# Optimization experiments

Hardware: AMD Instinct MI355X
Metric: run time of the kernel (lower is better)

Reference implementation:

```python
import jax, jax.numpy as jnp
import numpy as np

N = 4096   # node_each_graph == in_feats (adjacency-row node features)
H = 512    # n_hidden
C = 2      # n_classes
E = 65536  # edges (avg degree 16)
NL = 5     # n_layers -> 4 GINConv layers
NR = NL - 2  # stacked hidden GIN layers (layers 1..3)


def _bn(x, g, b, m, v):
    # BatchNorm1d in eval mode (running stats), eps=1e-5
    return (x - m) * jax.lax.rsqrt(v + 1e-5) * g + b


def setup_inputs():
    key = jax.random.key(0)
    ks = iter(jax.random.split(key, 16))
    nk = lambda: next(ks)
    s = 0.02
    f32 = jnp.float32
    d = {}
    d["feat"] = jax.random.normal(nk(), (N, N), f32)
    d["edge_src"] = jax.random.randint(nk(), (E,), 0, N)
    d["edge_dst"] = jax.random.randint(nk(), (E,), 0, N)
    # GIN layer 0: MLP is Linear(N,H)-BN-ReLU-Linear(H,H); ApplyNodeFunc BN; outer BN
    d["eps0"] = jnp.zeros((), f32)
    d["W0a"] = jax.random.normal(nk(), (N, H), f32) * s
    d["b0a"] = jnp.zeros((H,), f32)
    d["W0b"] = jax.random.normal(nk(), (H, H), f32) * s
    d["b0b"] = jnp.zeros((H,), f32)
    for nm in ["bn0a", "bnA0", "bnO0"]:
        d[nm + "_g"] = jnp.ones((H,), f32); d[nm + "_b"] = jnp.zeros((H,), f32)
        d[nm + "_m"] = jnp.zeros((H,), f32); d[nm + "_v"] = jnp.ones((H,), f32)
    # GIN layers 1..NL-2 stacked (H -> H)
    d["epsR"] = jnp.zeros((NR,), f32)
    d["WRa"] = jax.random.normal(nk(), (NR, H, H), f32) * s
    d["bRa"] = jnp.zeros((NR, H), f32)
    d["WRb"] = jax.random.normal(nk(), (NR, H, H), f32) * s
    d["bRb"] = jnp.zeros((NR, H), f32)
    for nm in ["bnRa", "bnAR", "bnOR"]:
        d[nm + "_g"] = jnp.ones((NR, H), f32); d[nm + "_b"] = jnp.zeros((NR, H), f32)
        d[nm + "_m"] = jnp.zeros((NR, H), f32); d[nm + "_v"] = jnp.ones((NR, H), f32)
    # per-hidden-rep readout linears (batch_size = 1)
    d["Wp0"] = jax.random.normal(nk(), (N * N, C), f32) * 0.001
    d["bp0"] = jnp.zeros((C,), f32)
    d["WpR"] = jax.random.normal(nk(), (NL - 1, N * H, C), f32) * 0.001
    d["bpR"] = jnp.zeros((NL - 1, C), f32)
    return d


def _gin(h, src, dst, eps, Wa, ba, bna, Wb, bb, bnA, bnO):
    # GINConv sum-aggregation: (1+eps)*h + sum over in-neighbors
    agg = jax.ops.segment_sum(h[src], dst, num_segments=N)
    x = (1.0 + eps) * h + agg
    # MLP (num_layers=2): Linear -> BN -> ReLU -> Linear
    x = jax.nn.relu(_bn(x @ Wa + ba, *bna))
    x = x @ Wb + bb
    # ApplyNodeFunc: BN -> ReLU
    x = jax.nn.relu(_bn(x, *bnA))
    # Model-level BN -> ReLU
    x = jax.nn.relu(_bn(x, *bnO))
    return x


def reference(feat, edge_src, edge_dst, eps0, W0a, b0a, W0b, b0b,
              bn0a_g, bn0a_b, bn0a_m, bn0a_v, bnA0_g, bnA0_b, bnA0_m, bnA0_v,
              bnO0_g, bnO0_b, bnO0_m, bnO0_v,
              epsR, WRa, bRa, WRb, bRb,
              bnRa_g, bnRa_b, bnRa_m, bnRa_v, bnAR_g, bnAR_b, bnAR_m, bnAR_v,
              bnOR_g, bnOR_b, bnOR_m, bnOR_v, Wp0, bp0, WpR, bpR):
    h = _gin(feat, edge_src, edge_dst, eps0, W0a, b0a,
             (bn0a_g, bn0a_b, bn0a_m, bn0a_v), W0b, b0b,
             (bnA0_g, bnA0_b, bnA0_m, bnA0_v), (bnO0_g, bnO0_b, bnO0_m, bnO0_v))
    hs = [h]
    for i in range(NR):  # small fixed layer loop
        h = _gin(h, edge_src, edge_dst, epsR[i], WRa[i], bRa[i],
                 (bnRa_g[i], bnRa_b[i], bnRa_m[i], bnRa_v[i]), WRb[i], bRb[i],
                 (bnAR_g[i], bnAR_b[i], bnAR_m[i], bnAR_v[i]),
                 (bnOR_g[i], bnOR_b[i], bnOR_m[i], bnOR_v[i]))
        hs.append(h)
    # jumping-knowledge readout over hidden_rep (eval: dropout = identity)
    score = feat.reshape(1, -1) @ Wp0 + bp0
    for i, hi in enumerate(hs):
        score = score + hi.reshape(1, -1) @ WpR[i] + bpR[i]
    return score
```

## Files before the change

kernel.cpp:

```cpp
#include <hip/hip_runtime.h>
#include <cstdint>
#include <cstddef>

typedef __attribute__((ext_vector_type(8))) short short8;
typedef __attribute__((ext_vector_type(4))) float f32x4;
typedef __attribute__((ext_vector_type(4))) float f4;
typedef __attribute__((ext_vector_type(2))) float f2;
typedef __attribute__((ext_vector_type(4))) unsigned short us4;

#define NN 4096
#define HH 512
#define EE 65536

#define GLOAD(gp, lp) __builtin_amdgcn_global_load_lds( \
    (const __attribute__((address_space(1))) void*)(gp), \
    (__attribute__((address_space(3))) void*)(lp), 16, 0, 0)

__device__ __forceinline__ unsigned short f2bf(float x) {
    union { float f; unsigned u; } un; un.f = x;
    unsigned r = un.u + 0x7fffu + ((un.u >> 16) & 1u);
    return (unsigned short)(r >> 16);
}
__device__ __forceinline__ float b2f(unsigned short v) {
    union { unsigned u; float f; } un; un.u = ((unsigned)v) << 16; return un.f;
}

__global__ __launch_bounds__(1024) void k_histscan(const int* __restrict__ edst,
                                                   int* __restrict__ starts) {
    __shared__ int cnt[NN];
    __shared__ int wtot[16], woff[16];
    const int t = threadIdx.x;
    for (int i = t; i < NN; i += 1024) cnt[i] = 0;
    __syncthreads();
    for (int i = t; i < EE; i += 1024) atomicAdd(&cnt[edst[i]], 1);
    __syncthreads();
    const int b = t * 4;
    const int c0 = cnt[b], c1 = cnt[b + 1], c2 = cnt[b + 2], c3 = cnt[b + 3];
    const int s = c0 + c1 + c2 + c3;
    const int lane = t & 63, wv = t >> 6;
    int inc = s;
    for (int d = 1; d < 64; d <<= 1) {
        int v = __shfl_up(inc, d);
        if (lane >= d) inc += v;
    }
    if (lane == 63) wtot[wv] = inc;
    __syncthreads();
    if (t == 0) {
        int a = 0;
        for (int i = 0; i < 16; ++i) { woff[i] = a; a += wtot[i]; }
        starts[NN] = a;
    }
    __syncthreads();
    int run = woff[wv] + inc - s;
    starts[b] = run; run += c0;
    starts[b + 1] = run; run += c1;
    starts[b + 2] = run; run += c2;
    starts[b + 3] = run;
}

__global__ void k_scatter(const int* __restrict__ src, const int* __restrict__ dst,
                          const int* __restrict__ starts, int* __restrict__ cursor,
                          int* __restrict__ sorted) {
    int e = blockIdx.x * 256 + threadIdx.x;
    if (e < EE) {
        int d = dst[e];
        int p = starts[d] + atomicAdd(&cursor[d], 1);
        sorted[p] = src[e];
    }
}

__global__ void k_binsort(const int* __restrict__ starts, int* __restrict__ a) {
    int d = blockIdx.x * 256 + threadIdx.x;
    if (d < NN) {
        int s = starts[d], e = starts[d + 1];
        for (int i = s + 1; i < e; ++i) {
            int v = a[i]; int j = i - 1;
            while (j >= s && a[j] > v) { a[j + 1] = a[j]; --j; }
            a[j + 1] = v;
        }
    }
}

__global__ __launch_bounds__(256) void k_cvtdot0(const float* __restrict__ feat,
                                                 const float* __restrict__ w,
                                                 unsigned short* __restrict__ featb,
                                                 float* __restrict__ part) {
    __shared__ f4 fs[1024];
    __shared__ float s0[256], s1[256];
    const int t = threadIdx.x;
    const long B0 = (long)blockIdx.x * 1024;
    const f4* ff = (const f4*)feat;
    const f4* ww = (const f4*)w;
    f4 v[4];
#pragma unroll
    for (int k = 0; k < 4; ++k)
        v[k] = __builtin_nontemporal_load(ff + B0 + k * 256 + t);
#pragma unroll
    for (int k = 0; k < 4; ++k) {
        fs[k * 256 + t] = v[k];
        us4 o;
        o.x = f2bf(v[k].x); o.y = f2bf(v[k].y); o.z = f2bf(v[k].z); o.w = f2bf(v[k].w);
        ((us4*)featb)[B0 + k * 256 + t] = o;
    }
    f4 wv[8];
#pragma unroll
    for (int k = 0; k < 8; ++k)
        wv[k] = __builtin_nontemporal_load(ww + 2 * B0 + k * 256 + t);
    __syncthreads();
    float a0 = 0.f, a1 = 0.f;
#pragma unroll
    for (int k = 0; k < 8; ++k) {
        const int q = k * 256 + t;
        f2 fp = *(const f2*)((const char*)fs + (size_t)q * 8);
        a0 += fp.x * wv[k].x + fp.y * wv[k].z;
        a1 += fp.x * wv[k].y + fp.y * wv[k].w;
    }
    s0[t] = a0; s1[t] = a1;
    __syncthreads();
    for (int s = 128; s > 0; s >>= 1) {
        if (t < s) { s0[t] += s0[t + s]; s1[t] += s1[t + s]; }
        __syncthreads();
    }
    if (t == 0) { part[2 * blockIdx.x] = s0[0]; part[2 * blockIdx.x + 1] = s1[0]; }
}

__global__ __launch_bounds__(256) void k_transcvt8(const float* __restrict__ W0a,
                                                   const float* __restrict__ W0b,
                                                   const float* __restrict__ WRa,
                                                   const float* __restrict__ WRb,
                                                   unsigned short* __restrict__ w0at,
                                                   unsigned short* __restrict__ wt) {
    __shared__ float tile[32][33];
    const int z = blockIdx.z;
    const float* W;
    unsigned short* Wt;
    int K;
    if (z == 7) {
        W = W0a; Wt = w0at; K = NN;
    } else {
        if (blockIdx.x >= 16 || blockIdx.y >= 16) return;
        W = (z == 0) ? W0b : (z < 4) ? WRa + (size_t)(z - 1) * HH * HH
                                     : WRb + (size_t)(z - 4) * HH * HH;
        Wt = wt + (size_t)z * HH * HH; K = HH;
    }
    const int k0 = blockIdx.x * 32, n0 = blockIdx.y * 32;
    const int tx = threadIdx.x & 31, ty = threadIdx.x >> 5;
    for (int r = ty; r < 32; r += 8)
        tile[r][tx] = W[(size_t)(k0 + r) * HH + n0 + tx];
    __syncthreads();
    for (int r = ty; r < 32; r += 8)
        Wt[(size_t)(n0 + r) * K + k0 + tx] = f2bf(tile[tx][r]);
}

__global__ __launch_bounds__(256) void k_gemm0(
    const unsigned short* __restrict__ A, const unsigned short* __restrict__ Bt,
    int M, int N, int K, float* __restrict__ outf)
{
    __shared__ alignas(16) unsigned short As[2][128 * 32];
    __shared__ alignas(16) unsigned short Bs[2][128 * 32];
    const int t = threadIdx.x;
    const int lane = t & 63, w = t >> 6;
    const int wr = w >> 1, wc = w & 1;
    const int l15 = lane & 15, l4 = lane >> 4;
    const int m0 = blockIdx.x * 128, n0 = blockIdx.y * 128;

    f32x4 acc[4][4];
#pragma unroll
    for (int i = 0; i < 4; ++i)
#pragma unroll
        for (int j = 0; j < 4; ++j) acc[i][j] = (f32x4){0.f, 0.f, 0.f, 0.f};

    const int Kc = K / gridDim.z;
    const int kbase = blockIdx.z * Kc;
    const unsigned short* ga0 = A + (size_t)m0 * K + kbase + (size_t)(t >> 2) * K + (t & 3) * 8;
    const unsigned short* ga1 = ga0 + (size_t)64 * K;
    const unsigned short* gb0 = Bt + (size_t)n0 * K + kbase + (size_t)(t >> 2) * K + (t & 3) * 8;
    const unsigned short* gb1 = gb0 + (size_t)64 * K;

    auto stage = [&](int kt, int buf) {
        const int ko = kt * 32;
        GLOAD(ga0 + ko, &As[buf][t * 8]);
        GLOAD(ga1 + ko, &As[buf][(t + 256) * 8]);
        GLOAD(gb0 + ko, &Bs[buf][t * 8]);
        GLOAD(gb1 + ko, &Bs[buf][(t + 256) * 8]);
    };

    const int nk = Kc >> 5;
    stage(0, 0);
    __syncthreads();
    for (int kt = 0; kt < nk; ++kt) {
        const int cur = kt & 1;
        if (kt + 1 < nk) stage(kt + 1, cur ^ 1);
        short8 aF[4], bF[4];
#pragma unroll
        for (int i = 0; i < 4; ++i)
            aF[i] = *(const short8*)(&As[cur][(wr * 64 + i * 16 + l15) * 32 + 8 * l4]);
#pragma unroll
        for (int j = 0; j < 4; ++j)
            bF[j] = *(const short8*)(&Bs[cur][(wc * 64 + j * 16 + l15) * 32 + 8 * l4]);
#pragma unroll
        for (int i = 0; i < 4; ++i)
#pragma unroll
            for (int j = 0; j < 4; ++j)
                acc[i][j] = __builtin_amdgcn_mfma_f32_16x16x32_bf16(aF[i], bF[j], acc[i][j], 0, 0, 0);
        __syncthreads();
    }

    const int mrow = m0 + wr * 64;
    float* op = outf + (size_t)blockIdx.z * M * N;
#pragma unroll
    for (int j = 0; j < 4; ++j) {
        const int cg = n0 + wc * 64 + j * 16 + l15;
#pragma unroll
        for (int i = 0; i < 4; ++i)
#pragma unroll
            for (int r = 0; r < 4; ++r)
                op[(size_t)(mrow + i * 16 + l4 * 4 + r) * N + cg] = acc[i][j][r];
    }
}

template<int EPI, bool DOT>
__global__ __launch_bounds__(512) void k_gemmH(
    const unsigned short* __restrict__ A, const unsigned short* __restrict__ Bt,
    const float* __restrict__ bias,
    const float* __restrict__ g1p, const float* __restrict__ b1p,
    const float* __restrict__ m1p, const float* __restrict__ v1p,
    const float* __restrict__ g2p, const float* __restrict__ b2p,
    const float* __restrict__ m2p, const float* __restrict__ v2p,
    unsigned short* __restrict__ outb,
    const float* __restrict__ wq, float* __restrict__ part, int slotbase)
{
    constexpr int K = HH, N = HH;
    __shared__ alignas(16) unsigned short As[2][128 * 32];
    __shared__ alignas(16) unsigned short Bs[2][64 * 32];
    const int t = threadIdx.x;
    const int lane = t & 63, w = t >> 6;
    const int wr = w >> 1, wc = w & 1;
    const int l15 = lane & 15, l4 = lane >> 4;
    const int m0 = blockIdx.x * 128, n0 = blockIdx.y * 64;

    f32x4 acc[2][2];
#pragma unroll
    for (int i = 0; i < 2; ++i)
#pragma unroll
        for (int j = 0; j < 2; ++j) acc[i][j] = (f32x4){0.f, 0.f, 0.f, 0.f};

    const unsigned short* ga = A + (size_t)m0 * K + (size_t)(t >> 2) * K + (t & 3) * 8;
    const unsigned short* gb = Bt + (size_t)n0 * K + (size_t)(t >> 2) * K + (t & 3) * 8;

    auto stage = [&](int kt, int buf) {
        const int ko = kt * 32;
        GLOAD(ga + ko, &As[buf][t * 8]);
        if (t < 256) GLOAD(gb + ko, &Bs[buf][t * 8]);
    };

    const int nk = K >> 5;
    stage(0, 0);
    __syncthreads();
    for (int kt = 0; kt < nk; ++kt) {
        const int cur = kt & 1;
        if (kt + 1 < nk) stage(kt + 1, cur ^ 1);
        short8 aF[2], bF[2];
#pragma unroll
        for (int i = 0; i < 2; ++i)
            aF[i] = *(const short8*)(&As[cur][(wr * 32 + i * 16 + l15) * 32 + 8 * l4]);
#pragma unroll
        for (int j = 0; j < 2; ++j)
            bF[j] = *(const short8*)(&Bs[cur][(wc * 32 + j * 16 + l15) * 32 + 8 * l4]);
#pragma unroll
        for (int i = 0; i < 2; ++i)
#pragma unroll
            for (int j = 0; j < 2; ++j)
                acc[i][j] = __builtin_amdgcn_mfma_f32_16x16x32_bf16(aF[i], bF[j], acc[i][j], 0, 0, 0);
        __syncthreads();
    }

    const int mrow = m0 + wr * 32;
    float d0 = 0.f, d1 = 0.f;
#pragma unroll
    for (int j = 0; j < 2; ++j) {
        const int cg = n0 + wc * 32 + j * 16 + l15;
        const float bi = bias[cg];
        const float sc1 = rsqrtf(v1p[cg] + 1e-5f) * g1p[cg];
        const float sh1 = b1p[cg] - m1p[cg] * sc1;
        float sc2 = 1.f, sh2 = 0.f;
        if (EPI == 3) {
            sc2 = rsqrtf(v2p[cg] + 1e-5f) * g2p[cg];
            sh2 = b2p[cg] - m2p[cg] * sc2;
        }
#pragma unroll
        for (int i = 0; i < 2; ++i) {
#pragma unroll
            for (int r = 0; r < 4; ++r) {
                const int rg = mrow + i * 16 + l4 * 4 + r;
                float x = acc[i][j][r];
                x = fmaxf((x + bi) * sc1 + sh1, 0.f);
                if (EPI == 3) x = fmaxf(x * sc2 + sh2, 0.f);
                outb[(size_t)rg * N + cg] = f2bf(x);
                if constexpr (DOT) {
                    float2 wvv = ((const float2*)wq)[(size_t)rg * N + cg];
                    d0 += x * wvv.x; d1 += x * wvv.y;
                }
            }
        }
    }
    if constexpr (DOT) {
        __shared__ float r0[512], r1[512];
        r0[t] = d0; r1[t] = d1;
        __syncthreads();
        for (int s = 256; s > 0; s >>= 1) {
            if (t < s) { r0[t] += r0[t + s]; r1[t] += r1[t + s]; }
            __syncthreads();
        }
        if (t == 0) {
            const int slot = slotbase + blockIdx.y * gridDim.x + blockIdx.x;
            part[2 * slot] = r0[0]; part[2 * slot + 1] = r1[0];
        }
    }
}

__global__ __launch_bounds__(256) void k_red4b(const float* __restrict__ p,
                                               unsigned short* __restrict__ G0b) {
    const long S = (long)NN * HH / 4;
    long i = blockIdx.x * 256L + threadIdx.x;
    float4 a = ((const float4*)p)[i];
    float4 b = ((const float4*)p)[i + S];
    float4 c = ((const float4*)p)[i + 2 * S];
    float4 d = ((const float4*)p)[i + 3 * S];
    us4 o;
    o.x = f2bf((a.x + b.x) + (c.x + d.x));
    o.y = f2bf((a.y + b.y) + (c.y + d.y));
    o.z = f2bf((a.z + b.z) + (c.z + d.z));
    o.w = f2bf((a.w + b.w) + (c.w + d.w));
    ((us4*)G0b)[i] = o;
}

__global__ __launch_bounds__(128) void k_agg0(
    const unsigned short* __restrict__ G0, const int* __restrict__ starts,
    const int* __restrict__ sorted, const float* __restrict__ epsp,
    const float* __restrict__ bias,
    const float* __restrict__ bg, const float* __restrict__ bb,
    const float* __restrict__ bm, const float* __restrict__ bv,
    unsigned short* __restrict__ outb)
{
    const int d = blockIdx.x, t = threadIdx.x;
    const float ep = 1.0f + epsp[0];
    ushort4 ow = ((const ushort4*)(G0 + (size_t)d * HH))[t];
    float sx = 0.f, sy = 0.f, sz = 0.f, sw = 0.f;
    const int e0 = starts[d], e1 = starts[d + 1];
    int i = e0;
    for (; i + 4 <= e1; i += 4) {
        int q0 = sorted[i], q1 = sorted[i + 1], q2 = sorted[i + 2], q3 = sorted[i + 3];
        ushort4 x0 = ((const ushort4*)(G0 + (size_t)q0 * HH))[t];
        ushort4 x1 = ((const ushort4*)(G0 + (size_t)q1 * HH))[t];
        ushort4 x2 = ((const ushort4*)(G0 + (size_t)q2 * HH))[t];
        ushort4 x3 = ((const ushort4*)(G0 + (size_t)q3 * HH))[t];
        sx += (b2f(x0.x) + b2f(x1.x)) + (b2f(x2.x) + b2f(x3.x));
        sy += (b2f(x0.y) + b2f(x1.y)) + (b2f(x2.y) + b2f(x3.y));
        sz += (b2f(x0.z) + b2f(x1.z)) + (b2f(x2.z) + b2f(x3.z));
        sw += (b2f(x0.w) + b2f(x1.w)) + (b2f(x2.w) + b2f(x3.w));
    }
    for (; i < e1; ++i) {
        ushort4 x = ((const ushort4*)(G0 + (size_t)sorted[i] * HH))[t];
        sx += b2f(x.x); sy += b2f(x.y); sz += b2f(x.z); sw += b2f(x.w);
    }
    float4 bi = ((const float4*)bias)[t];
    float4 g4 = ((const float4*)bg)[t];
    float4 b4 = ((const float4*)bb)[t];
    float4 m4 = ((const float4*)bm)[t];
    float4 v4 = ((const float4*)bv)[t];
    float x0 = ep * b2f(ow.x) + sx + bi.x;
    float x1 = ep * b2f(ow.y) + sy + bi.y;
    float x2 = ep * b2f(ow.z) + sz + bi.z;
    float x3 = ep * b2f(ow.w) + sw + bi.w;
    x0 = fmaxf((x0 - m4.x) * rsqrtf(v4.x + 1e-5f) * g4.x + b4.x, 0.f);
    x1 = fmaxf((x1 - m4.y) * rsqrtf(v4.y + 1e-5f) * g4.y + b4.y, 0.f);
    x2 = fmaxf((x2 - m4.z) * rsqrtf(v4.z + 1e-5f) * g4.z + b4.z, 0.f);
    x3 = fmaxf((x3 - m4.w) * rsqrtf(v4.w + 1e-5f) * g4.w + b4.w, 0.f);
    ushort4 o; o.x = f2bf(x0); o.y = f2bf(x1); o.z = f2bf(x2); o.w = f2bf(x3);
    ((ushort4*)(outb + (size_t)d * HH))[t] = o;
}

__global__ __launch_bounds__(128) void k_aggL(
    const unsigned short* __restrict__ hsrc, const int* __restrict__ starts,
    const int* __restrict__ sorted, const float* __restrict__ epsp,
    unsigned short* __restrict__ outb)
{
    const int d = blockIdx.x, t = threadIdx.x;
    const float ep = 1.0f + epsp[0];
    ushort4 ow = ((const ushort4*)(hsrc + (size_t)d * HH))[t];
    float sx = 0.f, sy = 0.f, sz = 0.f, sw = 0.f;
    const int e0 = starts[d], e1 = starts[d + 1];
    int i = e0;
    for (; i + 4 <= e1; i += 4) {
        int q0 = sorted[i], q1 = sorted[i + 1], q2 = sorted[i + 2], q3 = sorted[i + 3];
        ushort4 x0 = ((const ushort4*)(hsrc + (size_t)q0 * HH))[t];
        ushort4 x1 = ((const ushort4*)(hsrc + (size_t)q1 * HH))[t];
        ushort4 x2 = ((const ushort4*)(hsrc + (size_t)q2 * HH))[t];
        ushort4 x3 = ((const ushort4*)(hsrc + (size_t)q3 * HH))[t];
        sx += (b2f(x0.x) + b2f(x1.x)) + (b2f(x2.x) + b2f(x3.x));
        sy += (b2f(x0.y) + b2f(x1.y)) + (b2f(x2.y) + b2f(x3.y));
        sz += (b2f(x0.z) + b2f(x1.z)) + (b2f(x2.z) + b2f(x3.z));
        sw += (b2f(x0.w) + b2f(x1.w)) + (b2f(x2.w) + b2f(x3.w));
    }
    for (; i < e1; ++i) {
        ushort4 x = ((const ushort4*)(hsrc + (size_t)sorted[i] * HH))[t];
        sx += b2f(x.x); sy += b2f(x.y); sz += b2f(x.z); sw += b2f(x.w);
    }
    ushort4 o;
    o.x = f2bf(ep * b2f(ow.x) + sx);
    o.y = f2bf(ep * b2f(ow.y) + sy);
    o.z = f2bf(ep * b2f(ow.z) + sz);
    o.w = f2bf(ep * b2f(ow.w) + sw);
    ((ushort4*)(outb + (size_t)d * HH))[t] = o;
}

__global__ __launch_bounds__(256) void k_final(const float* __restrict__ part, int nslot,
                                               const float* __restrict__ bp0, const float* __restrict__ bpR,
                                               float* __restrict__ out) {
    __shared__ float s0[256], s1[256];
    int t = threadIdx.x;
    float a0 = 0.f, a1 = 0.f;
    for (int i = t; i < nslot; i += 256) { a0 += part[2 * i]; a1 += part[2 * i + 1]; }
    s0[t] = a0; s1[t] = a1;
    __syncthreads();
    for (int s = 128; s > 0; s >>= 1) {
        if (t < s) { s0[t] += s0[t + s]; s1[t] += s1[t + s]; }
        __syncthreads();
    }
    if (t == 0) {
        out[0] = s0[0] + bp0[0] + bpR[0] + bpR[2] + bpR[4] + bpR[6];
        out[1] = s1[0] + bp0[1] + bpR[1] + bpR[3] + bpR[5] + bpR[7];
    }
}

extern "C" void kernel_launch(void* const* d_in, const int* in_sizes, int n_in,
                              void* d_out, int out_size, void* d_ws, size_t ws_size,
                              hipStream_t stream)
{
    const float* feat = (const float*)d_in[0];
    const int*   esrc = (const int*)d_in[1];
    const int*   edst = (const int*)d_in[2];
    const float* eps0 = (const float*)d_in[3];
    const float* W0a  = (const float*)d_in[4];
    const float* b0a  = (const float*)d_in[5];
    const float* W0b  = (const float*)d_in[6];
    const float* b0b  = (const float*)d_in[7];
    const float* bn0a_g = (const float*)d_in[8];
    const float* bn0a_b = (const float*)d_in[9];
    const float* bn0a_m = (const float*)d_in[10];
    const float* bn0a_v = (const float*)d_in[11];
    const float* bnA0_g = (const float*)d_in[12];
    const float* bnA0_b = (const float*)d_in[13];
    const float* bnA0_m = (const float*)d_in[14];
    const float* bnA0_v = (const float*)d_in[15];
    const float* bnO0_g = (const float*)d_in[16];
    const float* bnO0_b = (const float*)d_in[17];
    const float* bnO0_m = (const float*)d_in[18];
    const float* bnO0_v = (const float*)d_in[19];
    const float* epsR = (const float*)d_in[20];
    const float* WRa  = (const float*)d_in[21];
    const float* bRa  = (const float*)d_in[22];
    const float* WRb  = (const float*)d_in[23];
    const float* bRb  = (const float*)d_in[24];
    const float* bnRa_g = (const float*)d_in[25];
    const float* bnRa_b = (const float*)d_in[26];
    const float* bnRa_m = (const float*)d_in[27];
    const float* bnRa_v = (const float*)d_in[28];
    const float* bnAR_g = (const float*)d_in[29];
    const float* bnAR_b = (const float*)d_in[30];
    const float* bnAR_m = (const float*)d_in[31];
    const float* bnAR_v = (const float*)d_in[32];
    const float* bnOR_g = (const float*)d_in[33];
    const float* bnOR_b = (const float*)d_in[34];
    const float* bnOR_m = (const float*)d_in[35];
    const float* bnOR_v = (const float*)d_in[36];
    const float* Wp0 = (const float*)d_in[37];
    const float* bp0 = (const float*)d_in[38];
    const float* WpR = (const float*)d_in[39];
    const float* bpR = (const float*)d_in[40];
    float* out = (float*)d_out;

    char* ws = (char*)d_ws;
    const size_t MB = 1024 * 1024;
    int*   starts = (int*)(ws + 0x10000);
    int*   cursor = (int*)(ws + 0x20000);
    int*   sorted = (int*)(ws + 0x30000);
    float* part   = (float*)(ws + 0x70000);
    unsigned short* featb = (unsigned short*)(ws + 1 * MB);
    unsigned short* w0at  = (unsigned short*)(ws + 33 * MB);
    unsigned short* wt    = (unsigned short*)(ws + 37 * MB);
    unsigned short* G0b   = (unsigned short*)(ws + 41 * MB);
    unsigned short* xb = (unsigned short*)(ws + 49 * MB);
    unsigned short* yb = (unsigned short*)(ws + 53 * MB);
    unsigned short* hb = (unsigned short*)(ws + 57 * MB);
    float* pbuf = (float*)(ws + 57 * MB);

    hipMemsetAsync(cursor, 0, NN * sizeof(int), stream);
    k_histscan<<<1, 1024, 0, stream>>>(edst, starts);
    k_scatter<<<EE / 256, 256, 0, stream>>>(esrc, edst, starts, cursor, sorted);
    k_binsort<<<NN / 256, 256, 0, stream>>>(starts, sorted);

    k_cvtdot0<<<4096, 256, 0, stream>>>(feat, Wp0, featb, part);
    k_transcvt8<<<dim3(NN / 32, HH / 32, 8), 256, 0, stream>>>(W0a, W0b, WRa, WRb, w0at, wt);

    k_gemm0<<<dim3(32, 4, 4), 256, 0, stream>>>(featb, w0at, NN, HH, NN, pbuf);
    k_red4b<<<2048, 256, 0, stream>>>(pbuf, G0b);
    k_agg0<<<NN, 128, 0, stream>>>(G0b, starts, sorted, eps0, b0a,
                                   bn0a_g, bn0a_b, bn0a_m, bn0a_v, xb);
    k_gemmH<3, true><<<dim3(32, 8), 512, 0, stream>>>(xb, wt,
        b0b, bnA0_g, bnA0_b, bnA0_m, bnA0_v, bnO0_g, bnO0_b, bnO0_m, bnO0_v,
        hb, WpR, part, 4096);

    for (int i = 0; i < 3; ++i) {
        const unsigned short* hp = hb + (size_t)i * NN * HH;
        unsigned short* hn = hb + (size_t)(i + 1) * NN * HH;
        k_aggL<<<NN, 128, 0, stream>>>(hp, starts, sorted, epsR + i, xb);
        k_gemmH<1, false><<<dim3(32, 8), 512, 0, stream>>>(xb, wt + (size_t)(1 + i) * HH * HH,
            bRa + (size_t)i * HH,
            bnRa_g + (size_t)i * HH, bnRa_b + (size_t)i * HH, bnRa_m + (size_t)i * HH, bnRa_v + (size_t)i * HH,
            nullptr, nullptr, nullptr, nullptr,
            yb, nullptr, nullptr, 0);
        k_gemmH<3, true><<<dim3(32, 8), 512, 0, stream>>>(yb, wt + (size_t)(4 + i) * HH * HH,
            bRb + (size_t)i * HH,
            bnAR_g + (size_t)i * HH, bnAR_b + (size_t)i * HH, bnAR_m + (size_t)i * HH, bnAR_v + (size_t)i * HH,
            bnOR_g + (size_t)i * HH, bnOR_b + (size_t)i * HH, bnOR_m + (size_t)i * HH, bnOR_v + (size_t)i * HH,
            hn, WpR + (size_t)(i + 1) * NN * HH * 2, part, 4096 + (i + 1) * 256);
    }

    k_final<<<1, 256, 0, stream>>>(part, 4096 + 4 * 256, bp0, bpR, out);
}
```

Measured before the change: 299.6 us.

## Unify GEMMs into one 64x64 BK64 kernel, drop split-K and fuse prep kernels

Replaces the split-K 128x128 layer-0 GEMM plus its fp32 reduction kernel with a single 64x64-tile kernel that writes bf16 directly, and uses the same tile kernel for all hidden GEMMs. It also merges the feature-convert/dot and weight-transpose kernels into one launch and folds the cursor memset into the histogram kernel. The aim is to cut launch count and the fp32 partial-sum traffic. The trade-off is a much longer per-block K loop for the 4096-deep GEMM and smaller tiles with less reuse.

```diff
diff --git a/kernel.cpp b/kernel.cpp
--- a/kernel.cpp
+++ b/kernel.cpp
@@ -26,11 +26,12 @@
 }
 
 __global__ __launch_bounds__(1024) void k_histscan(const int* __restrict__ edst,
-                                                   int* __restrict__ starts) {
+                                                   int* __restrict__ starts,
+                                                   int* __restrict__ cursor) {
     __shared__ int cnt[NN];
     __shared__ int wtot[16], woff[16];
     const int t = threadIdx.x;
-    for (int i = t; i < NN; i += 1024) cnt[i] = 0;
+    for (int i = t; i < NN; i += 1024) { cnt[i] = 0; cursor[i] = 0; }
     __syncthreads();
     for (int i = t; i < EE; i += 1024) atomicAdd(&cnt[edst[i]], 1);
     __syncthreads();
@@ -81,197 +82,143 @@
     }
 }
 
-__global__ __launch_bounds__(256) void k_cvtdot0(const float* __restrict__ feat,
-                                                 const float* __restrict__ w,
-                                                 unsigned short* __restrict__ featb,
-                                                 float* __restrict__ part) {
+__global__ __launch_bounds__(256) void k_prep(const float* __restrict__ feat,
+                                              const float* __restrict__ Wp0,
+                                              unsigned short* __restrict__ featb,
+                                              float* __restrict__ part,
+                                              const float* __restrict__ W0a,
+                                              const float* __restrict__ W0b,
+                                              const float* __restrict__ WRa,
+                                              const float* __restrict__ WRb,
+                                              unsigned short* __restrict__ w0at,
+                                              unsigned short* __restrict__ wt) {
     __shared__ f4 fs[1024];
     __shared__ float s0[256], s1[256];
+    __shared__ float tile[32][33];
     const int t = threadIdx.x;
-    const long B0 = (long)blockIdx.x * 1024;
-    const f4* ff = (const f4*)feat;
-    const f4* ww = (const f4*)w;
-    f4 v[4];
-#pragma unroll
-    for (int k = 0; k < 4; ++k)
-        v[k] = __builtin_nontemporal_load(ff + B0 + k * 256 + t);
-#pragma unroll
-    for (int k = 0; k < 4; ++k) {
-        fs[k * 256 + t] = v[k];
-        us4 o;
-        o.x = f2bf(v[k].x); o.y = f2bf(v[k].y); o.z = f2bf(v[k].z); o.w = f2bf(v[k].w);
-        ((us4*)featb)[B0 + k * 256 + t] = o;
-    }
-    f4 wv[8];
-#pragma unroll
-    for (int k = 0; k < 8; ++k)
-        wv[k] = __builtin_nontemporal_load(ww + 2 * B0 + k * 256 + t);
-    __syncthreads();
-    float a0 = 0.f, a1 = 0.f;
-#pragma unroll
-    for (int k = 0; k < 8; ++k) {
-        const int q = k * 256 + t;
-        f2 fp = *(const f2*)((const char*)fs + (size_t)q * 8);
-        a0 += fp.x * wv[k].x + fp.y * wv[k].z;
-        a1 += fp.x * wv[k].y + fp.y * wv[k].w;
-    }
-    s0[t] = a0; s1[t] = a1;
-    __syncthreads();
-    for (int s = 128; s > 0; s >>= 1) {
-        if (t < s) { s0[t] += s0[t + s]; s1[t] += s1[t + s]; }
-        __syncthreads();
-    }
-    if (t == 0) { part[2 * blockIdx.x] = s0[0]; part[2 * blockIdx.x + 1] = s1[0]; }
-}
-
-__global__ __launch_bounds__(256) void k_transcvt8(const float* __restrict__ W0a,
-                                                   const float* __restrict__ W0b,
-                                                   const float* __restrict__ WRa,
-                                                   const float* __restrict__ WRb,
-                                                   unsigned short* __restrict__ w0at,
-                                                   unsigned short* __restrict__ wt) {
-    __shared__ float tile[32][33];
-    const int z = blockIdx.z;
-    const float* W;
-    unsigned short* Wt;
-    int K;
-    if (z == 7) {
-        W = W0a; Wt = w0at; K = NN;
+    const int bid = blockIdx.x;
+    if (bid < 4096) {
+        const long B0 = (long)bid * 1024;
+        const f4* ff = (const f4*)feat;
+        const f4* ww = (const f4*)Wp0;
+        f4 v[4];
+#pragma unroll
+        for (int k = 0; k < 4; ++k)
+            v[k] = __builtin_nontemporal_load(ff + B0 + k * 256 + t);
+#pragma unroll
+        for (int k = 0; k < 4; ++k) {
+            fs[k * 256 + t] = v[k];
+            us4 o;
+            o.x = f2bf(v[k].x); o.y = f2bf(v[k].y); o.z = f2bf(v[k].z); o.w = f2bf(v[k].w);
+            __builtin_nontemporal_store(o, (us4*)featb + B0 + k * 256 + t);
+        }
+        f4 wv[8];
+#pragma unroll
+        for (int k = 0; k < 8; ++k)
+            wv[k] = __builtin_nontemporal_load(ww + 2 * B0 + k * 256 + t);
+        __syncthreads();
+        float a0 = 0.f, a1 = 0.f;
+#pragma unroll
+        for (int k = 0; k < 8; ++k) {
+            const int q = k * 256 + t;
+            f2 fp = *(const f2*)((const char*)fs + (size_t)q * 8);
+            a0 += fp.x * wv[k].x + fp.y * wv[k].z;
+            a1 += fp.x * wv[k].y + fp.y * wv[k].w;
+        }
+        s0[t] = a0; s1[t] = a1;
+        __syncthreads();
+        for (int s = 128; s > 0; s >>= 1) {
+            if (t < s) { s0[t] += s0[t + s]; s1[t] += s1[t + s]; }
+            __syncthreads();
+        }
+        if (t == 0) { part[2 * bid] = s0[0]; part[2 * bid + 1] = s1[0]; }
     } else {
-        if (blockIdx.x >= 16 || blockIdx.y >= 16) return;
-        W = (z == 0) ? W0b : (z < 4) ? WRa + (size_t)(z - 1) * HH * HH
-                                     : WRb + (size_t)(z - 4) * HH * HH;
-        Wt = wt + (size_t)z * HH * HH; K = HH;
-    }
-    const int k0 = blockIdx.x * 32, n0 = blockIdx.y * 32;
-    const int tx = threadIdx.x & 31, ty = threadIdx.x >> 5;
-    for (int r = ty; r < 32; r += 8)
-        tile[r][tx] = W[(size_t)(k0 + r) * HH + n0 + tx];
-    __syncthreads();
-    for (int r = ty; r < 32; r += 8)
-        Wt[(size_t)(n0 + r) * K + k0 + tx] = f2bf(tile[tx][r]);
-}
-
-__global__ __launch_bounds__(256) void k_gemm0(
-    const unsigned short* __restrict__ A, const unsigned short* __restrict__ Bt,
-    int M, int N, int K, float* __restrict__ outf)
+        const int tix = bid - 4096;
+        const float* W; unsigned short* Wt; int K, kb, nb;
+        if (tix < 2048) {
+            W = W0a; Wt = w0at; K = NN; kb = tix >> 4; nb = tix & 15;
+        } else {
+            const int t2 = tix - 2048;
+            const int z = t2 >> 8, r = t2 & 255;
+            W = (z == 0) ? W0b : (z < 4) ? WRa + (size_t)(z - 1) * HH * HH
+                                         : WRb + (size_t)(z - 4) * HH * HH;
+            Wt = wt + (size_t)z * HH * HH; K = HH; kb = r >> 4; nb = r & 15;
+        }
+        const int k0 = kb * 32, n0 = nb * 32;
+        const int tx = t & 31, ty = t >> 5;
+        for (int r = ty; r < 32; r += 8)
+            tile[r][tx] = W[(size_t)(k0 + r) * HH + n0 + tx];
+        __syncthreads();
+        for (int r = ty; r < 32; r += 8)
+            Wt[(size_t)(n0 + r) * K + k0 + tx] = f2bf(tile[tx][r]);
+    }
+}
+
+template<int EPI, bool DOT>
+__global__ __launch_bounds__(256) void k_gemmT(
+    const unsigned short* __restrict__ A, const unsigned short* __restrict__ Bt, int K,
+    const float* __restrict__ bias,
+    const float* __restrict__ g1, const float* __restrict__ b1,
+    const float* __restrict__ m1, const float* __restrict__ v1,
+    const float* __restrict__ g2, const float* __restrict__ b2,
+    const float* __restrict__ m2, const float* __restrict__ v2,
+    unsigned short* __restrict__ outb,
+    const float* __restrict__ wq, float* __restrict__ part, int slotbase)
 {
-    __shared__ alignas(16) unsigned short As[2][128 * 32];
-    __shared__ alignas(16) unsigned short Bs[2][128 * 32];
+    constexpr int N = HH;
+    __shared__ alignas(16) unsigned short As[2 * 4096];
+    __shared__ alignas(16) unsigned short Bs[2 * 4096];
     const int t = threadIdx.x;
     const int lane = t & 63, w = t >> 6;
     const int wr = w >> 1, wc = w & 1;
     const int l15 = lane & 15, l4 = lane >> 4;
-    const int m0 = blockIdx.x * 128, n0 = blockIdx.y * 128;
-
-    f32x4 acc[4][4];
-#pragma unroll
-    for (int i = 0; i < 4; ++i)
-#pragma unroll
-        for (int j = 0; j < 4; ++j) acc[i][j] = (f32x4){0.f, 0.f, 0.f, 0.f};
-
-    const int Kc = K / gridDim.z;
-    const int kbase = blockIdx.z * Kc;
-    const unsigned short* ga0 = A + (size_t)m0 * K + kbase + (size_t)(t >> 2) * K + (t & 3) * 8;
-    const unsigned short* ga1 = ga0 + (size_t)64 * K;
-    const unsigned short* gb0 = Bt + (size_t)n0 * K + kbase + (size_t)(t >> 2) * K + (t & 3) * 8;
-    const unsigned short* gb1 = gb0 + (size_t)64 * K;
+    const int m0 = blockIdx.x * 64, n0 = blockIdx.y * 64;
+
+    f32x4 acc[2][2];
+#pragma unroll
+    for (int i = 0; i < 2; ++i)
+#pragma unroll
+        for (int j = 0; j < 2; ++j) acc[i][j] = (f32x4){0.f, 0.f, 0.f, 0.f};
+
+    const unsigned short* ga0 = A + (size_t)(m0 + (t >> 3)) * K + (t & 7) * 8;
+    const unsigned short* ga1 = ga0 + (size_t)32 * K;
+    const unsigned short* gb0 = Bt + (size_t)(n0 + (t >> 3)) * K + (t & 7) * 8;
+    const unsigned short* gb1 = gb0 + (size_t)32 * K;
 
     auto stage = [&](int kt, int buf) {
-        const int ko = kt * 32;
-        GLOAD(ga0 + ko, &As[buf][t * 8]);
-        GLOAD(ga1 + ko, &As[buf][(t + 256) * 8]);
-        GLOAD(gb0 + ko, &Bs[buf][t * 8]);
-        GLOAD(gb1 + ko, &Bs[buf][(t + 256) * 8]);
+        const int ko = kt * 64;
+        GLOAD(ga0 + ko, As + buf * 4096 + t * 8);
+        GLOAD(ga1 + ko, As + buf * 4096 + 2048 + t * 8);
+        GLOAD(gb0 + ko, Bs + buf * 4096 + t * 8);
+        GLOAD(gb1 + ko, Bs + buf * 4096 + 2048 + t * 8);
     };
 
-    const int nk = Kc >> 5;
+    const int nk = K >> 6;
     stage(0, 0);
     __syncthreads();
     for (int kt = 0; kt < nk; ++kt) {
         const int cur = kt & 1;
         if (kt + 1 < nk) stage(kt + 1, cur ^ 1);
-        short8 aF[4], bF[4];
-#pragma unroll
-        for (int i = 0; i < 4; ++i)
-            aF[i] = *(const short8*)(&As[cur][(wr * 64 + i * 16 + l15) * 32 + 8 * l4]);
-#pragma unroll
-        for (int j = 0; j < 4; ++j)
-            bF[j] = *(const short8*)(&Bs[cur][(wc * 64 + j * 16 + l15) * 32 + 8 * l4]);
-#pragma unroll
-        for (int i = 0; i < 4; ++i)
-#pragma unroll
-            for (int j = 0; j < 4; ++j)
-                acc[i][j] = __builtin_amdgcn_mfma_f32_16x16x32_bf16(aF[i], bF[j], acc[i][j], 0, 0, 0);
-        __syncthreads();
-    }
-
-    const int mrow = m0 + wr * 64;
-    float* op = outf + (size_t)blockIdx.z * M * N;
-#pragma unroll
-    for (int j = 0; j < 4; ++j) {
-        const int cg = n0 + wc * 64 + j * 16 + l15;
-#pragma unroll
-        for (int i = 0; i < 4; ++i)
-#pragma unroll
-            for (int r = 0; r < 4; ++r)
-                op[(size_t)(mrow + i * 16 + l4 * 4 + r) * N + cg] = acc[i][j][r];
-    }
-}
-
-template<int EPI, bool DOT>
-__global__ __launch_bounds__(512) void k_gemmH(
-    const unsigned short* __restrict__ A, const unsigned short* __restrict__ Bt,
-    const float* __restrict__ bias,
-    const float* __restrict__ g1p, const float* __restrict__ b1p,
-    const float* __restrict__ m1p, const float* __restrict__ v1p,
-    const float* __restrict__ g2p, const float* __restrict__ b2p,
-    const float* __restrict__ m2p, const float* __restrict__ v2p,
-    unsigned short* __restrict__ outb,
-    const float* __restrict__ wq, float* __restrict__ part, int slotbase)
-{
-    constexpr int K = HH, N = HH;
-    __shared__ alignas(16) unsigned short As[2][128 * 32];
-    __shared__ alignas(16) unsigned short Bs[2][64 * 32];
-    const int t = threadIdx.x;
-    const int lane = t & 63, w = t >> 6;
-    const int wr = w >> 1, wc = w & 1;
-    const int l15 = lane & 15, l4 = lane >> 4;
-    const int m0 = blockIdx.x * 128, n0 = blockIdx.y * 64;
-
-    f32x4 acc[2][2];
-#pragma unroll
-    for (int i = 0; i < 2; ++i)
-#pragma unroll
-        for (int j = 0; j < 2; ++j) acc[i][j] = (f32x4){0.f, 0.f, 0.f, 0.f};
-
-    const unsigned short* ga = A + (size_t)m0 * K + (size_t)(t >> 2) * K + (t & 3) * 8;
-    const unsigned short* gb = Bt + (size_t)n0 * K + (size_t)(t >> 2) * K + (t & 3) * 8;
-
-    auto stage = [&](int kt, int buf) {
-        const int ko = kt * 32;
-        GLOAD(ga + ko, &As[buf][t * 8]);
-        if (t < 256) GLOAD(gb + ko, &Bs[buf][t * 8]);
-    };
-
-    const int nk = K >> 5;
-    stage(0, 0);
-    __syncthreads();
-    for (int kt = 0; kt < nk; ++kt) {
-        const int cur = kt & 1;
-        if (kt + 1 < nk) stage(kt + 1, cur ^ 1);
-        short8 aF[2], bF[2];
+        const unsigned short* Ac = As + cur * 4096;
+        const unsigned short* Bc = Bs + cur * 4096;
+        short8 aF[2][2], bF[2][2];
 #pragma unroll
         for (int i = 0; i < 2; ++i)
-            aF[i] = *(const short8*)(&As[cur][(wr * 32 + i * 16 + l15) * 32 + 8 * l4]);
+#pragma unroll
+            for (int ks = 0; ks < 2; ++ks)
+                aF[i][ks] = *(const short8*)(Ac + (wr * 32 + i * 16 + l15) * 64 + ks * 32 + l4 * 8);
 #pragma unroll
         for (int j = 0; j < 2; ++j)
-            bF[j] = *(const short8*)(&Bs[cur][(wc * 32 + j * 16 + l15) * 32 + 8 * l4]);
-#pragma unroll
-        for (int i = 0; i < 2; ++i)
-#pragma unroll
-            for (int j = 0; j < 2; ++j)
-                acc[i][j] = __builtin_amdgcn_mfma_f32_16x16x32_bf16(aF[i], bF[j], acc[i][j], 0, 0, 0);
+#pragma unroll
+            for (int ks = 0; ks < 2; ++ks)
+                bF[j][ks] = *(const short8*)(Bc + (wc * 32 + j * 16 + l15) * 64 + ks * 32 + l4 * 8);
+#pragma unroll
+        for (int ks = 0; ks < 2; ++ks)
+#pragma unroll
+            for (int i = 0; i < 2; ++i)
+#pragma unroll
+                for (int j = 0; j < 2; ++j)
+                    acc[i][j] = __builtin_amdgcn_mfma_f32_16x16x32_bf16(aF[i][ks], bF[j][ks], acc[i][j], 0, 0, 0);
         __syncthreads();
     }
 
@@ -280,13 +227,15 @@
 #pragma unroll
     for (int j = 0; j < 2; ++j) {
         const int cg = n0 + wc * 32 + j * 16 + l15;
-        const float bi = bias[cg];
-        const float sc1 = rsqrtf(v1p[cg] + 1e-5f) * g1p[cg];
-        const float sh1 = b1p[cg] - m1p[cg] * sc1;
-        float sc2 = 1.f, sh2 = 0.f;
+        float bi = 0.f, sc1 = 1.f, sh1 = 0.f, sc2 = 1.f, sh2 = 0.f;
+        if (EPI >= 1) {
+            bi = bias[cg];
+            sc1 = rsqrtf(v1[cg] + 1e-5f) * g1[cg];
+            sh1 = b1[cg] - m1[cg] * sc1;
+        }
         if (EPI == 3) {
-            sc2 = rsqrtf(v2p[cg] + 1e-5f) * g2p[cg];
-            sh2 = b2p[cg] - m2p[cg] * sc2;
+            sc2 = rsqrtf(v2[cg] + 1e-5f) * g2[cg];
+            sh2 = b2[cg] - m2[cg] * sc2;
         }
 #pragma unroll
         for (int i = 0; i < 2; ++i) {
@@ -294,21 +243,25 @@
             for (int r = 0; r < 4; ++r) {
                 const int rg = mrow + i * 16 + l4 * 4 + r;
                 float x = acc[i][j][r];
-                x = fmaxf((x + bi) * sc1 + sh1, 0.f);
-                if (EPI == 3) x = fmaxf(x * sc2 + sh2, 0.f);
+                if (EPI >= 1) {
+                    x = fmaxf((x + bi) * sc1 + sh1, 0.f);
+                    if (EPI == 3) x = fmaxf(x * sc2 + sh2, 0.f);
+                }
                 outb[(size_t)rg * N + cg] = f2bf(x);
                 if constexpr (DOT) {
-                    float2 wvv = ((const float2*)wq)[(size_t)rg * N + cg];
+                    f2 wvv = __builtin_nontemporal_load((const f2*)wq + (size_t)rg * N + cg);
                     d0 += x * wvv.x; d1 += x * wvv.y;
                 }
             }
         }
     }
     if constexpr (DOT) {
-        __shared__ float r0[512], r1[512];
+        float* r0 = (float*)As;
+        float* r1 = r0 + 256;
+        __syncthreads();
         r0[t] = d0; r1[t] = d1;
         __syncthreads();
-        for (int s = 256; s > 0; s >>= 1) {
+        for (int s = 128; s > 0; s >>= 1) {
             if (t < s) { r0[t] += r0[t + s]; r1[t] += r1[t + s]; }
             __syncthreads();
         }
@@ -317,22 +270,6 @@
             part[2 * slot] = r0[0]; part[2 * slot + 1] = r1[0];
         }
     }
-}
-
-__global__ __launch_bounds__(256) void k_red4b(const float* __restrict__ p,
-                                               unsigned short* __restrict__ G0b) {
-    const long S = (long)NN * HH / 4;
-    long i = blockIdx.x * 256L + threadIdx.x;
-    float4 a = ((const float4*)p)[i];
-    float4 b = ((const float4*)p)[i + S];
-    float4 c = ((const float4*)p)[i + 2 * S];
-    float4 d = ((const float4*)p)[i + 3 * S];
-    us4 o;
-    o.x = f2bf((a.x + b.x) + (c.x + d.x));
-    o.y = f2bf((a.y + b.y) + (c.y + d.y));
-    o.z = f2bf((a.z + b.z) + (c.z + d.z));
-    o.w = f2bf((a.w + b.w) + (c.w + d.w));
-    ((us4*)G0b)[i] = o;
 }
 
 __global__ __launch_bounds__(128) void k_agg0(
@@ -494,21 +431,22 @@
     unsigned short* xb = (unsigned short*)(ws + 49 * MB);
     unsigned short* yb = (unsigned short*)(ws + 53 * MB);
     unsigned short* hb = (unsigned short*)(ws + 57 * MB);
-    float* pbuf = (float*)(ws + 57 * MB);
-
-    hipMemsetAsync(cursor, 0, NN * sizeof(int), stream);
-    k_histscan<<<1, 1024, 0, stream>>>(edst, starts);
+
+    k_histscan<<<1, 1024, 0, stream>>>(edst, starts, cursor);
     k_scatter<<<EE / 256, 256, 0, stream>>>(esrc, edst, starts, cursor, sorted);
     k_binsort<<<NN / 256, 256, 0, stream>>>(starts, sorted);
 
-    k_cvtdot0<<<4096, 256, 0, stream>>>(feat, Wp0, featb, part);
-    k_transcvt8<<<dim3(NN / 32, HH / 32, 8), 256, 0, stream>>>(W0a, W0b, WRa, WRb, w0at, wt);
-
-    k_gemm0<<<dim3(32, 4, 4), 256, 0, stream>>>(featb, w0at, NN, HH, NN, pbuf);
-    k_red4b<<<2048, 256, 0, stream>>>(pbuf, G0b);
+    k_prep<<<4096 + 3840, 256, 0, stream>>>(feat, Wp0, featb, part,
+                                            W0a, W0b, WRa, WRb, w0at, wt);
+
+    const dim3 gg(NN / 64, HH / 64);
+
+    k_gemmT<0, false><<<gg, 256, 0, stream>>>(featb, w0at, NN,
+        nullptr, nullptr, nullptr, nullptr, nullptr, nullptr, nullptr, nullptr, nullptr,
+        G0b, nullptr, nullptr, 0);
     k_agg0<<<NN, 128, 0, stream>>>(G0b, starts, sorted, eps0, b0a,
                                    bn0a_g, bn0a_b, bn0a_m, bn0a_v, xb);
-    k_gemmH<3, true><<<dim3(32, 8), 512, 0, stream>>>(xb, wt,
+    k_gemmT<3, true><<<gg, 256, 0, stream>>>(xb, wt, HH,
         b0b, bnA0_g, bnA0_b, bnA0_m, bnA0_v, bnO0_g, bnO0_b, bnO0_m, bnO0_v,
         hb, WpR, part, 4096);
 
@@ -516,17 +454,17 @@
         const unsigned short* hp = hb + (size_t)i * NN * HH;
         unsigned short* hn = hb + (size_t)(i + 1) * NN * HH;
         k_aggL<<<NN, 128, 0, stream>>>(hp, starts, sorted, epsR + i, xb);
-        k_gemmH<1, false><<<dim3(32, 8), 512, 0, stream>>>(xb, wt + (size_t)(1 + i) * HH * HH,
+        k_gemmT<1, false><<<gg, 256, 0, stream>>>(xb, wt + (size_t)(1 + i) * HH * HH, HH,
             bRa + (size_t)i * HH,
             bnRa_g + (size_t)i * HH, bnRa_b + (size_t)i * HH, bnRa_m + (size_t)i * HH, bnRa_v + (size_t)i * HH,
             nullptr, nullptr, nullptr, nullptr,
             yb, nullptr, nullptr, 0);
-        k_gemmH<3, true><<<dim3(32, 8), 512, 0, stream>>>(yb, wt + (size_t)(4 + i) * HH * HH,
+        k_gemmT<3, true><<<gg, 256, 0, stream>>>(yb, wt + (size_t)(4 + i) * HH * HH, HH,
             bRb + (size_t)i * HH,
             bnAR_g + (size_t)i * HH, bnAR_b + (size_t)i * HH, bnAR_m + (size_t)i * HH, bnAR_v + (size_t)i * HH,
             bnOR_g + (size_t)i * HH, bnOR_b + (size_t)i * HH, bnOR_m + (size_t)i * HH, bnOR_v + (size_t)i * HH,
-            hn, WpR + (size_t)(i + 1) * NN * HH * 2, part, 4096 + (i + 1) * 256);
-    }
-
-    k_final<<<1, 256, 0, stream>>>(part, 4096 + 4 * 256, bp0, bpR, out);
-}
+            hn, WpR + (size_t)(i + 1) * NN * HH * 2, part, 4096 + (i + 1) * 512);
+    }
+
+    k_final<<<1, 256, 0, stream>>>(part, 4096 + 4 * 512, bp0, bpR, out);
+}
```

Measured after the change: 333.8 us. 11.4% more time.
